# Optimization experiments

Measured on AMD Instinct MI355X. Metric: run time of the kernel, lower is better.

Reference implementation:

```python
import jax, jax.numpy as jnp
import numpy as np

SUBDIV = 5      # icosphere subdivision level -> V = 10*4^5 + 2 = 10242
BATCH = 8
C_IN = 128
C_OUT = 128


def build_icosphere(n_sub):
    t = (1.0 + 5.0 ** 0.5) / 2.0
    verts = [np.array(v, dtype=np.float64) for v in [
        (-1, t, 0), (1, t, 0), (-1, -t, 0), (1, -t, 0),
        (0, -1, t), (0, 1, t), (0, -1, -t), (0, 1, -t),
        (t, 0, -1), (t, 0, 1), (-t, 0, -1), (-t, 0, 1)]]
    verts = [v / np.linalg.norm(v) for v in verts]
    faces = [(0, 11, 5), (0, 5, 1), (0, 1, 7), (0, 7, 10), (0, 10, 11),
             (1, 5, 9), (5, 11, 4), (11, 10, 2), (10, 7, 6), (7, 1, 8),
             (3, 9, 4), (3, 4, 2), (3, 2, 6), (3, 6, 8), (3, 8, 9),
             (4, 9, 5), (2, 4, 11), (6, 2, 10), (8, 6, 7), (9, 8, 1)]
    cache = {}

    def midpoint(a, b):
        key = (min(a, b), max(a, b))
        if key in cache:
            return cache[key]
        m = verts[a] + verts[b]
        m = m / np.linalg.norm(m)
        verts.append(m)
        cache[key] = len(verts) - 1
        return cache[key]

    for _ in range(n_sub):
        new_faces = []
        for a, b, c in faces:
            ab, bc, ca = midpoint(a, b), midpoint(b, c), midpoint(c, a)
            new_faces += [(a, ab, ca), (b, bc, ab), (c, ca, bc), (ab, bc, ca)]
        faces = new_faces
    edges = set()
    for a, b, c in faces:
        for u, v in ((a, b), (b, c), (c, a)):
            edges.add((min(u, v), max(u, v)))
    return np.stack(verts), sorted(edges)


def get_neighbors(nbr_vert, edges):
    nb = [[] for _ in range(nbr_vert)]
    for v1, v2 in edges:
        nb[v1].append(v2)
        nb[v2].append(v1)
    return nb


def sort_neighbors(nb):
    # walk the 1-ring so consecutive neighbors share an edge (same as torch code)
    out = []
    for i in range(len(nb)):
        rem = nb[i].copy()
        v = rem[0]
        s = [v]
        rem.remove(v)
        while rem:
            common = list(set(rem).intersection(nb[v]))
            v = common[0]
            s.append(v)
            rem.remove(v)
        out.append(s)
    return out


def sort_rotation(verts, nb):
    # orient the ring consistently (faithful to torch version incl. the >1 test)
    out = []
    for i, s in enumerate(nb):
        p0, p1, p2 = verts[i], verts[s[0]], verts[s[1]]
        v1 = p1 - p0
        v2 = p2 - p1
        vn = np.cross(v1, v2)
        n = vn / np.linalg.norm(vn)
        cg = p0 + 2.0 * ((p1 + v2 / 2.0) - p0) / 3.0
        out.append(list(s) if float(np.dot(n, cg)) > 1.0 else list(reversed(s)))
    return out


def build_patch_index():
    verts, edges = build_icosphere(SUBDIV)
    nb = sort_rotation(verts, sort_neighbors(get_neighbors(len(verts), edges)))
    V = len(verts)
    idx = np.zeros((V, 9), dtype=np.int32)
    mask = np.zeros((V, 9), dtype=np.float32)
    for i, ring in enumerate(nb):
        idx[i, 0] = i          # mat[i][i*9] = 1 -> self at slot 0
        mask[i, 0] = 1.0
        for j, v in enumerate(ring):  # neighbor j at slot j+1
            idx[i, j + 1] = v
            mask[i, j + 1] = 1.0
    return idx, mask


def setup_inputs() -> dict:
    idx, mask = build_patch_index()
    V = idx.shape[0]
    key = jax.random.key(0)
    k1, k2, k3 = jax.random.split(key, 3)
    x = jax.random.normal(k1, (BATCH, V, C_IN), dtype=jnp.float32)
    w = jax.random.normal(k2, (C_OUT, C_IN, 3, 3), dtype=jnp.float32) / np.sqrt(C_IN * 9.0)
    b = jax.random.normal(k3, (C_OUT,), dtype=jnp.float32) * 0.01
    return {"x": x, "w": w, "b": b,
            "nbr_idx": jnp.asarray(idx), "nbr_mask": jnp.asarray(mask)}


def reference(x, w, b, nbr_idx, nbr_mask):
    # x: [B, V, C]. The torch mm with the one-hot mat_neighbors is exactly a
    # gather of (self + up-to-6 ring neighbors) into a 3x3 patch, zero-padded.
    patches = x[:, nbr_idx, :] * nbr_mask[None, :, :, None]   # [B, V, 9, C]
    wk = w.reshape(C_OUT, C_IN, 9)                            # 3x3 kernel, valid conv on 3x3 patch
    out = jnp.einsum('bvkc,ock->bvo', patches, wk) + b        # [B, V, C_OUT]
    return out
```

## Files before the change

kernel.cpp:

```cpp
#include <hip/hip_runtime.h>
#include <hip/hip_bf16.h>


#define V_CNT    10242
#define CC       128
#define KS_ACT   7
#define BM       128
#define VT_PER_B 81
#define BATCH    8

typedef short short8 __attribute__((ext_vector_type(8)));
typedef float f32x4  __attribute__((ext_vector_type(4)));

__device__ __forceinline__ unsigned f2bf(float f) {
    unsigned u = __float_as_uint(f);
    u += 0x7fffu + ((u >> 16) & 1u);
    return u >> 16;
}

#define XB_OFF 0
#define WB_OFF 20975616
#define ZP_OFF 21204992

__global__ void wprep_kernel(const float* __restrict__ w, unsigned short* __restrict__ wb,
                             unsigned short* __restrict__ zp) {
    int i = blockIdx.x * 256 + threadIdx.x;
    if (i < 128 && blockIdx.x == 0) zp[i] = 0;
    if (i >= KS_ACT * CC * CC) return;
    int k = i >> 14;
    int r = i & 16383;
    int o = r >> 7;
    int c = r & 127;
    wb[i] = (unsigned short)f2bf(w[(o * CC + c) * 9 + k]);
}

__global__ void xprep_kernel(const float* __restrict__ x, unsigned short* __restrict__ xb, int n8) {
    int i = blockIdx.x * 256 + threadIdx.x;
    if (i >= n8) return;
    const float4* s = (const float4*)(x + (size_t)i * 8);
    float4 a = s[0], b = s[1];
    uint4 p;
    p.x = f2bf(a.x) | (f2bf(a.y) << 16);
    p.y = f2bf(a.z) | (f2bf(a.w) << 16);
    p.z = f2bf(b.x) | (f2bf(b.y) << 16);
    p.w = f2bf(b.z) | (f2bf(b.w) << 16);
    *(uint4*)(xb + (size_t)i * 8) = p;
}

__global__ __launch_bounds__(256, 3)
void icoconv_kernel(const unsigned short* __restrict__ xb,
                    const unsigned short* __restrict__ wb,
                    const unsigned short* __restrict__ zp,
                    const float* __restrict__ bias,
                    const int* __restrict__ nidx,
                    const float* __restrict__ nmask,
                    float* __restrict__ out) {
    __shared__ __align__(16) char smem[64 * 132 * 4];
    unsigned short* As = (unsigned short*)smem;
    float* Os = (float*)smem;

    const int tid  = threadIdx.x;
    const int lane = tid & 63;
    const int wid  = tid >> 6;
    const int bb   = blockIdx.x / VT_PER_B;
    const int vt   = blockIdx.x - bb * VT_PER_B;
    const int vbase = vt * BM;

    const int sr = tid >> 1;
    const int sh = tid & 1;
    const int v  = vbase + sr;
    const bool valid = v < V_CNT;

    int gidx[KS_ACT];
    unsigned mbits = 0;
    #pragma unroll
    for (int k = 0; k < KS_ACT; ++k) {
        int g = 0; float mk = 0.f;
        if (valid) { g = nidx[v * 9 + k]; mk = nmask[v * 9 + k]; }
        gidx[k] = g;
        mbits |= (mk != 0.f ? 1u : 0u) << k;
    }
    const unsigned short* xbatch = xb + (size_t)bb * V_CNT * CC;

    const int wave_m = wid >> 1;
    const int wave_n = wid & 1;

    f32x4 acc[4][4];
    #pragma unroll
    for (int i = 0; i < 4; ++i)
        #pragma unroll
        for (int j = 0; j < 4; ++j)
            acc[i][j] = f32x4{0.f, 0.f, 0.f, 0.f};

    const unsigned short* wlane = wb + (wave_n * 64 + (lane & 15)) * CC + ((lane >> 4) << 3);

    char* awr = (char*)As + sr * 256;
    const int swz = (sr & 7) << 4;

    uint4 pf[8];
    {
        const unsigned short* s = ((mbits & 1u) ? (xbatch + (size_t)gidx[0] * CC) : zp) + sh * 64;
        #pragma unroll
        for (int q = 0; q < 8; ++q) pf[q] = *(const uint4*)(s + q * 8);
    }

    for (int ks = 0; ks < KS_ACT; ++ks) {
        __syncthreads();
        #pragma unroll
        for (int q = 0; q < 8; ++q) {
            int w = sh * 8 + q;
            *(uint4*)(awr + ((w * 16) ^ swz)) = pf[q];
        }
        if (ks + 1 < KS_ACT) {
            const unsigned short* s =
                (((mbits >> (ks + 1)) & 1u) ? (xbatch + (size_t)gidx[ks + 1] * CC) : zp) + sh * 64;
            #pragma unroll
            for (int q = 0; q < 8; ++q) pf[q] = *(const uint4*)(s + q * 8);
        }
        __syncthreads();

        const unsigned short* wks = wlane + ks * (CC * CC);
        #pragma unroll
        for (int kk = 0; kk < 4; ++kk) {
            short8 bfr[4], af[4];
            #pragma unroll
            for (int ni = 0; ni < 4; ++ni)
                bfr[ni] = *(const short8*)(wks + ni * 16 * CC + kk * 32);
            #pragma unroll
            for (int mi = 0; mi < 4; ++mi) {
                int row = wave_m * 64 + mi * 16 + (lane & 15);
                af[mi] = *(const short8*)((const char*)As + row * 256 +
                          ((kk * 64 + ((lane >> 4) << 4)) ^ ((row & 7) << 4)));
            }
            #pragma unroll
            for (int mi = 0; mi < 4; ++mi)
                #pragma unroll
                for (int ni = 0; ni < 4; ++ni)
                    acc[mi][ni] = __builtin_amdgcn_mfma_f32_16x16x32_bf16(af[mi], bfr[ni], acc[mi][ni], 0, 0, 0);
        }
    }

    __syncthreads();
    const int r8 = tid >> 5;
    const int c4 = (tid & 31) << 2;
    float4 bv = *(const float4*)(bias + c4);

    #pragma unroll
    for (int pass = 0; pass < 2; ++pass) {
        if (wave_m == pass) {
            #pragma unroll
            for (int mi = 0; mi < 4; ++mi) {
                int lrow = mi * 16 + ((lane >> 4) << 2);
                #pragma unroll
                for (int ni = 0; ni < 4; ++ni) {
                    int lcol = wave_n * 64 + ni * 16 + (lane & 15);
                    #pragma unroll
                    for (int j = 0; j < 4; ++j)
                        Os[(lrow + j) * 132 + lcol] = acc[mi][ni][j];
                }
            }
        }
        __syncthreads();
        #pragma unroll
        for (int it = 0; it < 8; ++it) {
            int r = it * 8 + r8;
            int vv = vbase + pass * 64 + r;
            if (vv < V_CNT) {
                float4 val = *(const float4*)(Os + r * 132 + c4);
                val.x += bv.x; val.y += bv.y; val.z += bv.z; val.w += bv.w;
                *(float4*)(out + ((size_t)bb * V_CNT + vv) * CC + c4) = val;
            }
        }
        __syncthreads();
    }
}

extern "C" void kernel_launch(void* const* d_in, const int* in_sizes, int n_in,
                              void* d_out, int out_size, void* d_ws, size_t ws_size,
                              hipStream_t stream) {
    const float* x     = (const float*)d_in[0];
    const float* w     = (const float*)d_in[1];
    const float* bias  = (const float*)d_in[2];
    const int*   nidx  = (const int*)d_in[3];
    const float* nmask = (const float*)d_in[4];
    float* out = (float*)d_out;

    unsigned short* xb = (unsigned short*)((char*)d_ws + XB_OFF);
    unsigned short* wb = (unsigned short*)((char*)d_ws + WB_OFF);
    unsigned short* zp = (unsigned short*)((char*)d_ws + ZP_OFF);

    wprep_kernel<<<(KS_ACT * CC * CC + 255) / 256, 256, 0, stream>>>(w, wb, zp);

    int n8 = BATCH * V_CNT * CC / 8;
    xprep_kernel<<<(n8 + 255) / 256, 256, 0, stream>>>(x, xb, n8);

    icoconv_kernel<<<BATCH * VT_PER_B, 256, 0, stream>>>(xb, wb, zp, bias, nidx, nmask, out);
}
```

Baseline: 197.7 us.

## Halve vertex tile, double-buffer gathered patches, and fuse prep kernels

Cuts the vertex tile from 128 to 64 rows, which doubles the number of blocks. Each wave now owns 32 output channels across all 64 rows. The gathered input rows are double-buffered in shared memory with a two-step register prefetch, so only one barrier is needed per neighbor slot, and weight fragments are loaded before the A-fragment reads. The weight and input bf16 conversion kernels are merged into one launch, and the epilogue writes each output row in a single pass with nontemporal stores. Smaller tiles mean each weight fragment is reused across fewer rows, which raises weight traffic per output.

```diff
diff --git a/kernel.cpp b/kernel.cpp
--- a/kernel.cpp
+++ b/kernel.cpp
@@ -5,8 +5,8 @@
 #define V_CNT    10242
 #define CC       128
 #define KS_ACT   7
-#define BM       128
-#define VT_PER_B 81
+#define BM       64
+#define VT_PER_B 161
 #define BATCH    8
 
 typedef short short8 __attribute__((ext_vector_type(8)));
@@ -22,29 +22,35 @@
 #define WB_OFF 20975616
 #define ZP_OFF 21204992
 
-__global__ void wprep_kernel(const float* __restrict__ w, unsigned short* __restrict__ wb,
-                             unsigned short* __restrict__ zp) {
-    int i = blockIdx.x * 256 + threadIdx.x;
-    if (i < 128 && blockIdx.x == 0) zp[i] = 0;
-    if (i >= KS_ACT * CC * CC) return;
-    int k = i >> 14;
-    int r = i & 16383;
-    int o = r >> 7;
-    int c = r & 127;
-    wb[i] = (unsigned short)f2bf(w[(o * CC + c) * 9 + k]);
-}
-
-__global__ void xprep_kernel(const float* __restrict__ x, unsigned short* __restrict__ xb, int n8) {
-    int i = blockIdx.x * 256 + threadIdx.x;
-    if (i >= n8) return;
-    const float4* s = (const float4*)(x + (size_t)i * 8);
-    float4 a = s[0], b = s[1];
-    uint4 p;
-    p.x = f2bf(a.x) | (f2bf(a.y) << 16);
-    p.y = f2bf(a.z) | (f2bf(a.w) << 16);
-    p.z = f2bf(b.x) | (f2bf(b.y) << 16);
-    p.w = f2bf(b.z) | (f2bf(b.w) << 16);
-    *(uint4*)(xb + (size_t)i * 8) = p;
+#define XB_BLOCKS 5121
+#define WB_BLOCKS 448
+
+__global__ void prep_kernel(const float* __restrict__ x, const float* __restrict__ w,
+                            unsigned short* __restrict__ xb, unsigned short* __restrict__ wb,
+                            unsigned short* __restrict__ zp, int n8) {
+    int b = blockIdx.x;
+    if (b < XB_BLOCKS) {
+        int i = b * 256 + threadIdx.x;
+        if (i < n8) {
+            const float4* s = (const float4*)(x + (size_t)i * 8);
+            float4 a = s[0], c = s[1];
+            uint4 p;
+            p.x = f2bf(a.x) | (f2bf(a.y) << 16);
+            p.y = f2bf(a.z) | (f2bf(a.w) << 16);
+            p.z = f2bf(c.x) | (f2bf(c.y) << 16);
+            p.w = f2bf(c.z) | (f2bf(c.w) << 16);
+            *(uint4*)(xb + (size_t)i * 8) = p;
+        }
+    } else if (b < XB_BLOCKS + WB_BLOCKS) {
+        int i = (b - XB_BLOCKS) * 256 + threadIdx.x;
+        int k = i >> 14;
+        int r = i & 16383;
+        int o = r >> 7;
+        int c = r & 127;
+        wb[i] = (unsigned short)f2bf(w[(o * CC + c) * 9 + k]);
+    } else {
+        if (threadIdx.x < 128) zp[threadIdx.x] = 0;
+    }
 }
 
 __global__ __launch_bounds__(256, 3)
@@ -56,7 +62,8 @@
                     const float* __restrict__ nmask,
                     float* __restrict__ out) {
     __shared__ __align__(16) char smem[64 * 132 * 4];
-    unsigned short* As = (unsigned short*)smem;
+    unsigned short* As0 = (unsigned short*)smem;
+    unsigned short* As1 = (unsigned short*)(smem + 16384);
     float* Os = (float*)smem;
 
     const int tid  = threadIdx.x;
@@ -66,8 +73,8 @@
     const int vt   = blockIdx.x - bb * VT_PER_B;
     const int vbase = vt * BM;
 
-    const int sr = tid >> 1;
-    const int sh = tid & 1;
+    const int sr = tid >> 2;
+    const int sh = tid & 3;
     const int v  = vbase + sr;
     const bool valid = v < V_CNT;
 
@@ -82,96 +89,112 @@
     }
     const unsigned short* xbatch = xb + (size_t)bb * V_CNT * CC;
 
-    const int wave_m = wid >> 1;
-    const int wave_n = wid & 1;
-
-    f32x4 acc[4][4];
+    f32x4 acc[4][2];
     #pragma unroll
     for (int i = 0; i < 4; ++i)
         #pragma unroll
-        for (int j = 0; j < 4; ++j)
+        for (int j = 0; j < 2; ++j)
             acc[i][j] = f32x4{0.f, 0.f, 0.f, 0.f};
 
-    const unsigned short* wlane = wb + (wave_n * 64 + (lane & 15)) * CC + ((lane >> 4) << 3);
-
-    char* awr = (char*)As + sr * 256;
-    const int swz = (sr & 7) << 4;
-
-    uint4 pf[8];
-    {
-        const unsigned short* s = ((mbits & 1u) ? (xbatch + (size_t)gidx[0] * CC) : zp) + sh * 64;
-        #pragma unroll
-        for (int q = 0; q < 8; ++q) pf[q] = *(const uint4*)(s + q * 8);
-    }
-
-    for (int ks = 0; ks < KS_ACT; ++ks) {
-        __syncthreads();
-        #pragma unroll
-        for (int q = 0; q < 8; ++q) {
-            int w = sh * 8 + q;
-            *(uint4*)(awr + ((w * 16) ^ swz)) = pf[q];
-        }
-        if (ks + 1 < KS_ACT) {
+    const unsigned short* wlane = wb + (wid * 32 + (lane & 15)) * CC + ((lane >> 4) << 3);
+
+    const int swz  = (sr & 7) << 4;
+    const int hi16 = (lane >> 4) << 4;
+
+    uint4 pf[4];
+    {
+        const unsigned short* s = ((mbits & 1u) ? (xbatch + (size_t)gidx[0] * CC) : zp) + sh * 32;
+        #pragma unroll
+        for (int q = 0; q < 4; ++q) pf[q] = *(const uint4*)(s + q * 8);
+    }
+    {
+        char* wdst = (char*)As0 + sr * 256;
+        #pragma unroll
+        for (int q = 0; q < 4; ++q)
+            *(uint4*)(wdst + ((sh * 64 + q * 16) ^ swz)) = pf[q];
+    }
+    {
+        const unsigned short* s = (((mbits >> 1) & 1u) ? (xbatch + (size_t)gidx[1] * CC) : zp) + sh * 32;
+        #pragma unroll
+        for (int q = 0; q < 4; ++q) pf[q] = *(const uint4*)(s + q * 8);
+    }
+    __syncthreads();
+
+    #pragma unroll
+    for (int t = 0; t < KS_ACT; ++t) {
+        const unsigned short* bcur = (t & 1) ? As1 : As0;
+        unsigned short*       bnxt = (t & 1) ? As0 : As1;
+
+        if (t < KS_ACT - 1) {
+            char* wdst = (char*)bnxt + sr * 256;
+            #pragma unroll
+            for (int q = 0; q < 4; ++q)
+                *(uint4*)(wdst + ((sh * 64 + q * 16) ^ swz)) = pf[q];
+        }
+
+        const unsigned short* wks = wlane + t * (CC * CC);
+        short8 bfr[4][2];
+        #pragma unroll
+        for (int kk = 0; kk < 4; ++kk)
+            #pragma unroll
+            for (int ni = 0; ni < 2; ++ni)
+                bfr[kk][ni] = *(const short8*)(wks + ni * 16 * CC + kk * 32);
+
+        if (t < KS_ACT - 2) {
+            const int k2 = t + 2;
             const unsigned short* s =
-                (((mbits >> (ks + 1)) & 1u) ? (xbatch + (size_t)gidx[ks + 1] * CC) : zp) + sh * 64;
-            #pragma unroll
-            for (int q = 0; q < 8; ++q) pf[q] = *(const uint4*)(s + q * 8);
-        }
-        __syncthreads();
-
-        const unsigned short* wks = wlane + ks * (CC * CC);
+                (((mbits >> k2) & 1u) ? (xbatch + (size_t)gidx[k2] * CC) : zp) + sh * 32;
+            #pragma unroll
+            for (int q = 0; q < 4; ++q) pf[q] = *(const uint4*)(s + q * 8);
+        }
+
         #pragma unroll
         for (int kk = 0; kk < 4; ++kk) {
-            short8 bfr[4], af[4];
-            #pragma unroll
-            for (int ni = 0; ni < 4; ++ni)
-                bfr[ni] = *(const short8*)(wks + ni * 16 * CC + kk * 32);
+            short8 af[4];
             #pragma unroll
             for (int mi = 0; mi < 4; ++mi) {
-                int row = wave_m * 64 + mi * 16 + (lane & 15);
-                af[mi] = *(const short8*)((const char*)As + row * 256 +
-                          ((kk * 64 + ((lane >> 4) << 4)) ^ ((row & 7) << 4)));
+                int row = mi * 16 + (lane & 15);
+                af[mi] = *(const short8*)((const char*)bcur + row * 256 +
+                          ((kk * 64 + hi16) ^ ((row & 7) << 4)));
             }
             #pragma unroll
             for (int mi = 0; mi < 4; ++mi)
                 #pragma unroll
-                for (int ni = 0; ni < 4; ++ni)
-                    acc[mi][ni] = __builtin_amdgcn_mfma_f32_16x16x32_bf16(af[mi], bfr[ni], acc[mi][ni], 0, 0, 0);
-        }
+                for (int ni = 0; ni < 2; ++ni)
+                    acc[mi][ni] = __builtin_amdgcn_mfma_f32_16x16x32_bf16(af[mi], bfr[kk][ni], acc[mi][ni], 0, 0, 0);
+        }
+
+        if (t < KS_ACT - 1) __syncthreads();
     }
 
     __syncthreads();
-    const int r8 = tid >> 5;
-    const int c4 = (tid & 31) << 2;
-    float4 bv = *(const float4*)(bias + c4);
-
-    #pragma unroll
-    for (int pass = 0; pass < 2; ++pass) {
-        if (wave_m == pass) {
-            #pragma unroll
-            for (int mi = 0; mi < 4; ++mi) {
-                int lrow = mi * 16 + ((lane >> 4) << 2);
-                #pragma unroll
-                for (int ni = 0; ni < 4; ++ni) {
-                    int lcol = wave_n * 64 + ni * 16 + (lane & 15);
-                    #pragma unroll
-                    for (int j = 0; j < 4; ++j)
-                        Os[(lrow + j) * 132 + lcol] = acc[mi][ni][j];
-                }
+    #pragma unroll
+    for (int mi = 0; mi < 4; ++mi) {
+        int lrow = mi * 16 + ((lane >> 4) << 2);
+        #pragma unroll
+        for (int ni = 0; ni < 2; ++ni) {
+            int lcol = wid * 32 + ni * 16 + (lane & 15);
+            #pragma unroll
+            for (int j = 0; j < 4; ++j)
+                Os[(lrow + j) * 132 + lcol] = acc[mi][ni][j];
+        }
+    }
+    __syncthreads();
+
+    {
+        const int r  = tid >> 2;
+        const int cb = (tid & 3) << 5;
+        const int vv = vbase + r;
+        if (vv < V_CNT) {
+            float* op = out + ((size_t)bb * V_CNT + vv) * CC + cb;
+            #pragma unroll
+            for (int q = 0; q < 8; ++q) {
+                f32x4 val = *(const f32x4*)(Os + r * 132 + cb + q * 4);
+                f32x4 bv  = *(const f32x4*)(bias + cb + q * 4);
+                val = val + bv;
+                __builtin_nontemporal_store(val, (f32x4*)(op + q * 4));
             }
         }
-        __syncthreads();
-        #pragma unroll
-        for (int it = 0; it < 8; ++it) {
-            int r = it * 8 + r8;
-            int vv = vbase + pass * 64 + r;
-            if (vv < V_CNT) {
-                float4 val = *(const float4*)(Os + r * 132 + c4);
-                val.x += bv.x; val.y += bv.y; val.z += bv.z; val.w += bv.w;
-                *(float4*)(out + ((size_t)bb * V_CNT + vv) * CC + c4) = val;
-            }
-        }
-        __syncthreads();
     }
 }
 
@@ -189,10 +212,8 @@
     unsigned short* wb = (unsigned short*)((char*)d_ws + WB_OFF);
     unsigned short* zp = (unsigned short*)((char*)d_ws + ZP_OFF);
 
-    wprep_kernel<<<(KS_ACT * CC * CC + 255) / 256, 256, 0, stream>>>(w, wb, zp);
-
     int n8 = BATCH * V_CNT * CC / 8;
-    xprep_kernel<<<(n8 + 255) / 256, 256, 0, stream>>>(x, xb, n8);
+    prep_kernel<<<XB_BLOCKS + WB_BLOCKS + 1, 256, 0, stream>>>(x, w, xb, wb, zp, n8);
 
     icoconv_kernel<<<BATCH * VT_PER_B, 256, 0, stream>>>(xb, wb, zp, bias, nidx, nmask, out);
 }
```

Result: faster. 193.7 us (-2.0%).
